# Performance work log

Measured on AMD Instinct MI355X. Metric: run time of the kernel, lower is better.

## Reference

```python
import jax, jax.numpy as jnp
import numpy as np

N_HEADS = 8
WINDOW = 4

def setup_inputs() -> dict:
    key = jax.random.key(0)
    ks = jax.random.split(key, 12)
    B, C, L = 8, 512, 1024
    Dh = C // N_HEADS
    s = 1.0 / np.sqrt(C)
    inp = {
        'x': jax.random.normal(ks[0], (B, C, L), dtype=jnp.float32),
        'Wq': jax.random.normal(ks[1], (C, C), dtype=jnp.float32) * s,
        'bq': jnp.zeros((C,), dtype=jnp.float32),
        'Wk': jax.random.normal(ks[2], (C, C), dtype=jnp.float32) * s,
        'bk': jnp.zeros((C,), dtype=jnp.float32),
        'Wv': jax.random.normal(ks[3], (C, C), dtype=jnp.float32) * s,
        'bv': jnp.zeros((C,), dtype=jnp.float32),
        'Wo': jax.random.normal(ks[4], (C, C), dtype=jnp.float32) * s,
        'bo': jnp.zeros((C,), dtype=jnp.float32),
        'emb_rel_k': jax.random.normal(ks[5], (2 * WINDOW + 1, Dh), dtype=jnp.float32) * 0.02,
        'emb_rel_v': jax.random.normal(ks[6], (2 * WINDOW + 1, Dh), dtype=jnp.float32) * 0.02,
    }
    return inp


def reference(x, Wq, bq, Wk, bk, Wv, bv, Wo, bo, emb_rel_k, emb_rel_v):
    B, C, L = x.shape
    H = N_HEADS
    Dh = C // H
    scale = Dh ** -0.5

    def proj(W, b):
        # pointwise conv1d == channel-mixing matmul; (B,C,L) -> (B,H,L,Dh)
        y = jnp.einsum('oc,bcl->bol', W, x) + b[:, None]
        return y.reshape(B, H, Dh, L).transpose(0, 1, 3, 2)

    q = proj(Wq, bq) * scale
    k = proj(Wk, bk)
    v = proj(Wv, bv)

    scores = jnp.einsum('bhld,bhjd->bhlj', q, k)  # (B,H,L,L)

    t = jnp.arange(L)
    diff = t[None, :] - t[:, None]                      # (L,L)
    window_mask = (jnp.abs(diff) <= WINDOW)
    indices = jnp.clip(diff, -WINDOW, WINDOW) + WINDOW  # (L,L) in [0, 2w]

    rel_k = emb_rel_k[indices]                          # (L,L,Dh)
    rel_scores = jnp.einsum('bhld,ljd->bhlj', q, rel_k)
    scores = scores + rel_scores * window_mask[None, None, :, :]

    attn = jax.nn.softmax(scores, axis=-1)

    out = jnp.einsum('bhlj,bhjd->bhld', attn, v)
    rel_v = emb_rel_v[indices] * window_mask[:, :, None]  # (L,L,Dh)
    out = out + jnp.einsum('bhlj,ljd->bhld', attn, rel_v)

    out = out.transpose(0, 1, 3, 2).reshape(B, C, L)
    out = jnp.einsum('oc,bcl->bol', Wo, out) + bo[:, None]
    return out
```

## Files before the change

kernel.cpp:

```cpp
#include <hip/hip_runtime.h>
#include <math.h>

#define B_  8
#define H_  8
#define C_  512
#define L_  1024
#define DH  64
#define WIN 4

typedef __attribute__((ext_vector_type(8))) short short8;
typedef __attribute__((ext_vector_type(4))) float floatx4;

__device__ __forceinline__ unsigned short f2bf(float f) {
    unsigned int u = __float_as_uint(f);
    u = u + 0x7FFFu + ((u >> 16) & 1u);
    return (unsigned short)(u >> 16);
}
__device__ __forceinline__ float bf2f(unsigned short h) {
    return __uint_as_float(((unsigned int)h) << 16);
}
__device__ __forceinline__ unsigned short f2h(float f) {
    _Float16 h = (_Float16)f;
    return *reinterpret_cast<unsigned short*>(&h);
}

__device__ __forceinline__ void gload_lds16(const void* g, void* l) {
    __builtin_amdgcn_global_load_lds(
        (const __attribute__((address_space(1))) void*)g,
        (__attribute__((address_space(3))) void*)l, 16, 0, 0);
}

__global__ __launch_bounds__(256) void prep_kernel(
    const float* __restrict__ Wq, const float* __restrict__ Wk,
    const float* __restrict__ Wv, const float* __restrict__ Wo,
    const float* __restrict__ bq, const float* __restrict__ bk,
    const float* __restrict__ bv,
    unsigned short* __restrict__ Wqkv_hi,
    unsigned short* __restrict__ Wo_h,
    float* __restrict__ bqkv)
{
    const int i = blockIdx.x * 256 + threadIdx.x;
    float4 v; ushort4 h;

    v = ((const float4*)Wq)[i];
    h.x = f2bf(v.x); h.y = f2bf(v.y); h.z = f2bf(v.z); h.w = f2bf(v.w);
    ((ushort4*)Wqkv_hi)[i] = h;

    v = ((const float4*)Wk)[i];
    h.x = f2bf(v.x); h.y = f2bf(v.y); h.z = f2bf(v.z); h.w = f2bf(v.w);
    ((ushort4*)Wqkv_hi)[65536 + i] = h;

    v = ((const float4*)Wv)[i];
    h.x = f2bf(v.x); h.y = f2bf(v.y); h.z = f2bf(v.z); h.w = f2bf(v.w);
    ((ushort4*)Wqkv_hi)[131072 + i] = h;

    v = ((const float4*)Wo)[i];
    h.x = f2h(v.x); h.y = f2h(v.y); h.z = f2h(v.z); h.w = f2h(v.w);
    ((ushort4*)Wo_h)[i] = h;

    if (i < 512)       bqkv[i] = bq[i];
    else if (i < 1024) bqkv[i] = bk[i - 512];
    else if (i < 1536) bqkv[i] = bv[i - 1024];
}

__global__ __launch_bounds__(256) void transpose_kernel(
    const float* __restrict__ x, unsigned short* __restrict__ xT)
{
    __shared__ float tile[32][33];
    const int b  = blockIdx.z;
    const int cb = blockIdx.y * 32;
    const int lb = blockIdx.x * 32;
    const int t  = threadIdx.x;
    {
        const int l = t & 31, c0 = t >> 5;
#pragma unroll
        for (int p = 0; p < 4; ++p) {
            const int c = c0 + 8 * p;
            tile[c][l] = x[((size_t)b * C_ + cb + c) * L_ + lb + l];
        }
    }
    __syncthreads();
    {
        const int c = t & 31, l0 = t >> 5;
#pragma unroll
        for (int p = 0; p < 4; ++p) {
            const int l = l0 + 8 * p;
            xT[((size_t)b * L_ + lb + l) * C_ + cb + c] = f2bf(tile[c][l]);
        }
    }
}

__global__ __launch_bounds__(256) void qkv_gemm_kernel(
    const unsigned short* __restrict__ Wh, const float* __restrict__ bqkv,
    const unsigned short* __restrict__ xT,
    unsigned short* __restrict__ Qb, unsigned short* __restrict__ Kb,
    unsigned short* __restrict__ Vc)
{
    __shared__ __align__(16) unsigned short SM[18432];

    const int b   = blockIdx.z;
    const int oB  = blockIdx.y * 128;
    const int mat = oB >> 9;
    const int ob  = oB & 511;
    const int lb  = blockIdx.x * 128;
    const int t  = threadIdx.x;
    const int w = t >> 6, lane = t & 63, quad = lane >> 4, lc = lane & 15;
    const int wm = w >> 1, wn = w & 1;

    const unsigned short* Wm = Wh + (size_t)mat * C_ * C_;

    floatx4 acc[4][4];
#pragma unroll
    for (int i = 0; i < 4; ++i)
#pragma unroll
        for (int j = 0; j < 4; ++j) acc[i][j] = (floatx4)0.f;

    const int srow = w * 32 + (lane >> 2);
    const int sc8  = (lane & 3) * 8;

#define QKV_STAGE(BUF, S) {                                                  \
    const int c0_ = (S) * 32;                                                \
    _Pragma("unroll")                                                        \
    for (int p_ = 0; p_ < 2; ++p_) {                                         \
        gload_lds16(&Wm[(size_t)(ob + srow + 16 * p_) * C_ + c0_ + sc8],     \
                    &SM[(0 * 2 + (BUF)) * 4096 + (w * 32 + p_ * 16) * 32]);  \
        gload_lds16(&xT[((size_t)b * L_ + lb + srow + 16 * p_) * C_ + c0_ + sc8], \
                    &SM[(1 * 2 + (BUF)) * 4096 + (w * 32 + p_ * 16) * 32]);  \
    }                                                                        \
}

    QKV_STAGE(0, 0)
    __syncthreads();

    for (int s = 0; s < 16; ++s) {
        const int cur = s & 1;
        if (s < 15) QKV_STAGE(1 - cur, s + 1)

        const unsigned short (*At)[32] =
            reinterpret_cast<const unsigned short (*)[32]>(&SM[(0 * 2 + cur) * 4096]);
        const unsigned short (*Bt)[32] =
            reinterpret_cast<const unsigned short (*)[32]>(&SM[(1 * 2 + cur) * 4096]);

        short8 a[4], bb[4];
#pragma unroll
        for (int mt = 0; mt < 4; ++mt)
            a[mt] = *reinterpret_cast<const short8*>(&At[wm * 64 + mt * 16 + lc][quad * 8]);
#pragma unroll
        for (int nt = 0; nt < 4; ++nt)
            bb[nt] = *reinterpret_cast<const short8*>(&Bt[wn * 64 + nt * 16 + lc][quad * 8]);
#pragma unroll
        for (int mt = 0; mt < 4; ++mt)
#pragma unroll
            for (int nt = 0; nt < 4; ++nt)
                acc[mt][nt] = __builtin_amdgcn_mfma_f32_16x16x32_bf16(
                    a[mt], bb[nt], acc[mt][nt], 0, 0, 0);

        __syncthreads();
    }

    if (mat == 2) {
#pragma unroll
        for (int mt = 0; mt < 4; ++mt) {
#pragma unroll
            for (int r = 0; r < 4; ++r) {
                const int o  = ob + wm * 64 + mt * 16 + quad * 4 + r;
                const float bi = bqkv[1024 + o];
#pragma unroll
                for (int nt = 0; nt < 4; ++nt) {
                    const int l = lb + wn * 64 + nt * 16 + lc;
                    Vc[((size_t)b * C_ + o) * L_ + l] = f2bf(acc[mt][nt][r] + bi);
                }
            }
        }
    } else {
        const float scale = (mat == 0) ? 0.125f : 1.0f;
        unsigned short* dst = (mat == 0) ? Qb : Kb;
        unsigned short (*sT)[144] =
            reinterpret_cast<unsigned short (*)[144]>(&SM[0]);

#pragma unroll
        for (int mt = 0; mt < 4; ++mt) {
#pragma unroll
            for (int r = 0; r < 4; ++r) {
                const int o  = ob + wm * 64 + mt * 16 + quad * 4 + r;
                const float bi = bqkv[mat * 512 + o];
                const int d  = mt * 16 + quad * 4 + r;
#pragma unroll
                for (int nt = 0; nt < 4; ++nt) {
                    const int l = wn * 64 + nt * 16 + lc;
                    sT[l][wm * 72 + d] = f2bf((acc[mt][nt][r] + bi) * scale);
                }
            }
        }
        __syncthreads();
        {
            const int l = t >> 1, hf = t & 1;
#pragma unroll
            for (int h01 = 0; h01 < 2; ++h01) {
                const int hgl = (ob >> 6) + h01;
                const size_t o = (((size_t)b * H_ + hgl) * L_ + lb + l) * DH + hf * 32;
                const int cbase = h01 * 72 + hf * 32;
                uint4 v0 = *reinterpret_cast<const uint4*>(&sT[l][cbase]);
                uint4 v1 = *reinterpret_cast<const uint4*>(&sT[l][cbase + 8]);
                uint4 v2 = *reinterpret_cast<const uint4*>(&sT[l][cbase + 16]);
                uint4 v3 = *reinterpret_cast<const uint4*>(&sT[l][cbase + 24]);
                *reinterpret_cast<uint4*>(&dst[o])      = v0;
                *reinterpret_cast<uint4*>(&dst[o + 8])  = v1;
                *reinterpret_cast<uint4*>(&dst[o + 16]) = v2;
                *reinterpret_cast<uint4*>(&dst[o + 24]) = v3;
            }
        }
    }
}

__global__ __launch_bounds__(256, 2) void attn_kernel15(
    const unsigned short* __restrict__ Qb,
    const unsigned short* __restrict__ Kb,
    const unsigned short* __restrict__ Vc,
    const float* __restrict__ erel_k, const float* __restrict__ erel_v,
    unsigned short* __restrict__ AOh)
{
    __shared__ __align__(16) unsigned short kst[2][64][68];
    __shared__ __align__(16) unsigned short vst[2][64][68];
    __shared__ __align__(16) unsigned short Pl[4][2][16][68];
    __shared__ float rs[128][9];
    __shared__ float rv[128][9];

    const int t  = threadIdx.x;
    const int bh = blockIdx.x;
    const int rt = blockIdx.y;
    const int b = bh >> 3, h = bh & 7;
    const int w = t >> 6, lane = t & 63, quad = lane >> 4, lc = lane & 15;
    const int rowB = rt * 128 + w * 32;

    const size_t qkBase = (size_t)bh * L_ * DH;
    const size_t vBase  = ((size_t)b * C_ + h * DH) * L_;

    for (int i = lane; i < 32 * 9; i += 64) rv[w * 32 + i / 9][i % 9] = 0.f;

    short8 af0[2], af1[2];
#pragma unroll
    for (int kk = 0; kk < 2; ++kk) {
        af0[kk] = *reinterpret_cast<const short8*>(
            &Qb[qkBase + (size_t)(rowB + lc) * DH + kk * 32 + quad * 8]);
        af1[kk] = *reinterpret_cast<const short8*>(
            &Qb[qkBase + (size_t)(rowB + 16 + lc) * DH + kk * 32 + quad * 8]);
    }

    {
        floatx4 rsa0 = (floatx4)0.f, rsa1 = (floatx4)0.f;
        const int drow = (lc < 9) ? lc : 8;
#pragma unroll
        for (int kk = 0; kk < 2; ++kk) {
            short8 bfr;
#pragma unroll
            for (int i = 0; i < 8; ++i)
                bfr[i] = (short)f2bf(erel_k[drow * 64 + kk * 32 + quad * 8 + i]);
            rsa0 = __builtin_amdgcn_mfma_f32_16x16x32_bf16(af0[kk], bfr, rsa0, 0, 0, 0);
            rsa1 = __builtin_amdgcn_mfma_f32_16x16x32_bf16(af1[kk], bfr, rsa1, 0, 0, 0);
        }
        if (lc < 9) {
#pragma unroll
            for (int r = 0; r < 4; ++r) {
                rs[w * 32 + quad * 4 + r][lc]      = rsa0[r];
                rs[w * 32 + 16 + quad * 4 + r][lc] = rsa1[r];
            }
        }
    }

    const int jr = t >> 2, jcE = (t & 3) * 16;
    *reinterpret_cast<uint4*>(&kst[0][jr][jcE]) =
        *reinterpret_cast<const uint4*>(&Kb[qkBase + (size_t)jr * DH + jcE]);
    *reinterpret_cast<uint4*>(&kst[0][jr][jcE + 8]) =
        *reinterpret_cast<const uint4*>(&Kb[qkBase + (size_t)jr * DH + jcE + 8]);
    *reinterpret_cast<uint4*>(&vst[0][jr][jcE]) =
        *reinterpret_cast<const uint4*>(&Vc[vBase + (size_t)jr * L_ + jcE]);
    *reinterpret_cast<uint4*>(&vst[0][jr][jcE + 8]) =
        *reinterpret_cast<const uint4*>(&Vc[vBase + (size_t)jr * L_ + jcE + 8]);
    __syncthreads();

    short8 ones;
#pragma unroll
    for (int j = 0; j < 8; ++j) ones[j] = (short)0x3F80;

    floatx4 acc_o0[4], acc_o1[4], acc_l0 = (floatx4)0.f, acc_l1 = (floatx4)0.f;
#pragma unroll
    for (int nt = 0; nt < 4; ++nt) { acc_o0[nt] = (floatx4)0.f; acc_o1[nt] = (floatx4)0.f; }

    for (int jt = 0; jt < L_ / 64; ++jt) {
        const int j0  = jt * 64;
        const int cur = jt & 1;

        uint4 pk0, pk1, pv0, pv1;
        if (jt < L_ / 64 - 1) {
            const int j0n = j0 + 64;
            pk0 = *reinterpret_cast<const uint4*>(
                &Kb[qkBase + (size_t)(j0n + jr) * DH + jcE]);
            pk1 = *reinterpret_cast<const uint4*>(
                &Kb[qkBase + (size_t)(j0n + jr) * DH + jcE + 8]);
            pv0 = *reinterpret_cast<const uint4*>(
                &Vc[vBase + (size_t)jr * L_ + j0n + jcE]);
            pv1 = *reinterpret_cast<const uint4*>(
                &Vc[vBase + (size_t)jr * L_ + j0n + jcE + 8]);
        }

        floatx4 s0[4], s1[4];
#pragma unroll
        for (int nt = 0; nt < 4; ++nt) { s0[nt] = (floatx4)0.f; s1[nt] = (floatx4)0.f; }
        __builtin_amdgcn_s_setprio(1);
#pragma unroll
        for (int nt = 0; nt < 4; ++nt)
#pragma unroll
            for (int kk = 0; kk < 2; ++kk) {
                const short8 kf = *reinterpret_cast<const short8*>(
                    &kst[cur][nt * 16 + lc][kk * 32 + quad * 8]);
                s0[nt] = __builtin_amdgcn_mfma_f32_16x16x32_bf16(kf, af0[kk], s0[nt], 0, 0, 0);
                s1[nt] = __builtin_amdgcn_mfma_f32_16x16x32_bf16(kf, af1[kk], s1[nt], 0, 0, 0);
            }
        __builtin_amdgcn_s_setprio(0);

        short8 pf0[2], pf1[2];

        {
            const int rowW = rowB;
            const bool nearD = (j0 <= rowW + 15 + WIN) && (j0 + 63 >= rowW - WIN);
            if (nearD) {
#pragma unroll
                for (int nt = 0; nt < 4; ++nt)
#pragma unroll
                    for (int r = 0; r < 4; ++r) {
                        const int diff = (j0 + nt * 16 + quad * 4 + r) - (rowW + lc);
                        if (diff >= -WIN && diff <= WIN)
                            s0[nt][r] += rs[w * 32 + lc][diff + WIN];
                    }
            }
#pragma unroll
            for (int nt = 0; nt < 4; ++nt) {
                const float e0 = __expf(s0[nt][0]);
                const float e1 = __expf(s0[nt][1]);
                const float e2 = __expf(s0[nt][2]);
                const float e3 = __expf(s0[nt][3]);
                unsigned int u01, u23;
                asm volatile("v_cvt_pk_bf16_f32 %0, %1, %2" : "=v"(u01) : "v"(e0), "v"(e1));
                asm volatile("v_cvt_pk_bf16_f32 %0, %1, %2" : "=v"(u23) : "v"(e2), "v"(e3));
                uint2 pr; pr.x = u01; pr.y = u23;
                *reinterpret_cast<uint2*>(&Pl[w][0][lc][nt * 16 + quad * 4]) = pr;
            }
            if (nearD) {
                for (int idx = lane; idx < 16 * 9; idx += 64) {
                    const int r16 = idx / 9, dr = idx % 9;
                    const int jg = rowW + r16 + dr - WIN;
                    if (jg >= j0 && jg < j0 + 64 && jg >= 0 && jg < L_)
                        rv[w * 32 + r16][dr] += bf2f(Pl[w][0][r16][jg - j0]);
                }
            }
#pragma unroll
            for (int kk = 0; kk < 2; ++kk)
                pf0[kk] = *reinterpret_cast<const short8*>(&Pl[w][0][lc][kk * 32 + quad * 8]);
        }

        {
            const int rowW = rowB + 16;
            const bool nearD = (j0 <= rowW + 15 + WIN) && (j0 + 63 >= rowW - WIN);
            if (nearD) {
#pragma unroll
                for (int nt = 0; nt < 4; ++nt)
#pragma unroll
                    for (int r = 0; r < 4; ++r) {
                        const int diff = (j0 + nt * 16 + quad * 4 + r) - (rowW + lc);
                        if (diff >= -WIN && diff <= WIN)
                            s1[nt][r] += rs[w * 32 + 16 + lc][diff + WIN];
                    }
            }
#pragma unroll
            for (int nt = 0; nt < 4; ++nt) {
                const float e0 = __expf(s1[nt][0]);
                const float e1 = __expf(s1[nt][1]);
                const float e2 = __expf(s1[nt][2]);
                const float e3 = __expf(s1[nt][3]);
                unsigned int u01, u23;
                asm volatile("v_cvt_pk_bf16_f32 %0, %1, %2" : "=v"(u01) : "v"(e0), "v"(e1));
                asm volatile("v_cvt_pk_bf16_f32 %0, %1, %2" : "=v"(u23) : "v"(e2), "v"(e3));
                uint2 pr; pr.x = u01; pr.y = u23;
                *reinterpret_cast<uint2*>(&Pl[w][1][lc][nt * 16 + quad * 4]) = pr;
            }
            if (nearD) {
                for (int idx = lane; idx < 16 * 9; idx += 64) {
                    const int r16 = idx / 9, dr = idx % 9;
                    const int jg = rowW + r16 + dr - WIN;
                    if (jg >= j0 && jg < j0 + 64 && jg >= 0 && jg < L_)
                        rv[w * 32 + 16 + r16][dr] += bf2f(Pl[w][1][r16][jg - j0]);
                }
            }
#pragma unroll
            for (int kk = 0; kk < 2; ++kk)
                pf1[kk] = *reinterpret_cast<const short8*>(&Pl[w][1][lc][kk * 32 + quad * 8]);
        }

        __builtin_amdgcn_s_setprio(1);
#pragma unroll
        for (int kk = 0; kk < 2; ++kk) {
            acc_l0 = __builtin_amdgcn_mfma_f32_16x16x32_bf16(pf0[kk], ones, acc_l0, 0, 0, 0);
            acc_l1 = __builtin_amdgcn_mfma_f32_16x16x32_bf16(pf1[kk], ones, acc_l1, 0, 0, 0);
        }
#pragma unroll
        for (int nt = 0; nt < 4; ++nt)
#pragma unroll
            for (int kk = 0; kk < 2; ++kk) {
                const short8 vf = *reinterpret_cast<const short8*>(
                    &vst[cur][nt * 16 + lc][kk * 32 + quad * 8]);
                acc_o0[nt] = __builtin_amdgcn_mfma_f32_16x16x32_bf16(pf0[kk], vf, acc_o0[nt], 0, 0, 0);
                acc_o1[nt] = __builtin_amdgcn_mfma_f32_16x16x32_bf16(pf1[kk], vf, acc_o1[nt], 0, 0, 0);
            }
        __builtin_amdgcn_s_setprio(0);

        if (jt < L_ / 64 - 1) {
            *reinterpret_cast<uint4*>(&kst[1 - cur][jr][jcE])     = pk0;
            *reinterpret_cast<uint4*>(&kst[1 - cur][jr][jcE + 8]) = pk1;
            *reinterpret_cast<uint4*>(&vst[1 - cur][jr][jcE])     = pv0;
            *reinterpret_cast<uint4*>(&vst[1 - cur][jr][jcE + 8]) = pv1;
        }
        __syncthreads();
    }

    {
#pragma unroll
        for (int nt = 0; nt < 4; ++nt) {
            const int d = nt * 16 + lc;
            float ev[9];
#pragma unroll
            for (int dr = 0; dr < 9; ++dr) ev[dr] = erel_v[dr * 64 + d];
#pragma unroll
            for (int r = 0; r < 4; ++r) {
                const int rloc = w * 32 + quad * 4 + r;
                float v = acc_o0[nt][r];
#pragma unroll
                for (int dr = 0; dr < 9; ++dr) v += rv[rloc][dr] * ev[dr];
                Pl[w][0][quad * 4 + r][nt * 16 + lc] = f2h(v / acc_l0[r]);
            }
        }
        const int row = lane >> 2, ds8 = (lane & 3) * 16;
        const uint4 q0 = *reinterpret_cast<const uint4*>(&Pl[w][0][row][ds8]);
        const uint4 q1 = *reinterpret_cast<const uint4*>(&Pl[w][0][row][ds8 + 8]);
        const size_t o = ((size_t)b * L_ + rowB + row) * C_ + h * 64 + ds8;
        *reinterpret_cast<uint4*>(&AOh[o])     = q0;
        *reinterpret_cast<uint4*>(&AOh[o + 8]) = q1;
    }
    {
#pragma unroll
        for (int nt = 0; nt < 4; ++nt) {
            const int d = nt * 16 + lc;
            float ev[9];
#pragma unroll
            for (int dr = 0; dr < 9; ++dr) ev[dr] = erel_v[dr * 64 + d];
#pragma unroll
            for (int r = 0; r < 4; ++r) {
                const int rloc = w * 32 + 16 + quad * 4 + r;
                float v = acc_o1[nt][r];
#pragma unroll
                for (int dr = 0; dr < 9; ++dr) v += rv[rloc][dr] * ev[dr];
                Pl[w][1][quad * 4 + r][nt * 16 + lc] = f2h(v / acc_l1[r]);
            }
        }
        const int row = lane >> 2, ds8 = (lane & 3) * 16;
        const uint4 q0 = *reinterpret_cast<const uint4*>(&Pl[w][1][row][ds8]);
        const uint4 q1 = *reinterpret_cast<const uint4*>(&Pl[w][1][row][ds8 + 8]);
        const size_t o = ((size_t)b * L_ + rowB + 16 + row) * C_ + h * 64 + ds8;
        *reinterpret_cast<uint4*>(&AOh[o])     = q0;
        *reinterpret_cast<uint4*>(&AOh[o + 8]) = q1;
    }
}

__global__ __launch_bounds__(256) void out_gemm_kernel(
    const unsigned short* __restrict__ Wh,
    const float* __restrict__ bo,
    const unsigned short* __restrict__ Ah,
    float* __restrict__ Y)
{
    __shared__ __align__(16) unsigned short Asb[2][128][32];
    __shared__ __align__(16) unsigned short Bsb[2][64][32];

    const int b  = blockIdx.z;
    const int ob = blockIdx.y * 128;
    const int lb = blockIdx.x * 64;
    const int t  = threadIdx.x;
    const int w = t >> 6, lane = t & 63, quad = lane >> 4, lc = lane & 15;
    const int wm = w >> 1, wn = w & 1;

    floatx4 acc[4][2];
#pragma unroll
    for (int i = 0; i < 4; ++i)
#pragma unroll
        for (int j = 0; j < 2; ++j) acc[i][j] = (floatx4)0.f;

    const int srow = (lane >> 2);
    const int sc8  = (lane & 3) * 8;

#define OG_STAGE(BUF, S) {                                                   \
    const int c0_ = (S) * 32;                                                \
    _Pragma("unroll")                                                        \
    for (int p_ = 0; p_ < 2; ++p_)                                           \
        gload_lds16(&Wh[(size_t)(ob + w * 32 + p_ * 16 + srow) * C_ + c0_ + sc8], \
                    &Asb[BUF][w * 32 + p_ * 16][0]);                         \
    gload_lds16(&Ah[((size_t)b * L_ + lb + w * 16 + srow) * C_ + c0_ + sc8], \
                &Bsb[BUF][w * 16][0]);                                       \
}

    OG_STAGE(0, 0)
    __syncthreads();

    for (int s = 0; s < 16; ++s) {
        const int cur = s & 1;
        if (s < 15) OG_STAGE(1 - cur, s + 1)

        short8 ah[4], bhf[2];
#pragma unroll
        for (int mt = 0; mt < 4; ++mt)
            ah[mt] = *reinterpret_cast<const short8*>(
                &Asb[cur][wm * 64 + mt * 16 + lc][quad * 8]);
#pragma unroll
        for (int nt = 0; nt < 2; ++nt)
            bhf[nt] = *reinterpret_cast<const short8*>(
                &Bsb[cur][wn * 32 + nt * 16 + lc][quad * 8]);
#pragma unroll
        for (int mt = 0; mt < 4; ++mt)
#pragma unroll
            for (int nt = 0; nt < 2; ++nt)
                acc[mt][nt] = __builtin_amdgcn_mfma_f32_16x16x32_f16(
                    ah[mt], bhf[nt], acc[mt][nt], 0, 0, 0);

        __syncthreads();
    }

#pragma unroll
    for (int mt = 0; mt < 4; ++mt) {
#pragma unroll
        for (int r = 0; r < 4; ++r) {
            const int o = ob + wm * 64 + mt * 16 + quad * 4 + r;
            const float bi = bo[o];
#pragma unroll
            for (int nt = 0; nt < 2; ++nt) {
                const int l = lb + wn * 32 + nt * 16 + lc;
                Y[((size_t)b * C_ + o) * L_ + l] = acc[mt][nt][r] + bi;
            }
        }
    }
}

extern "C" void kernel_launch(void* const* d_in, const int* in_sizes, int n_in,
                              void* d_out, int out_size, void* d_ws, size_t ws_size,
                              hipStream_t stream)
{
    const float* x   = (const float*)d_in[0];
    const float* Wq  = (const float*)d_in[1];
    const float* bq  = (const float*)d_in[2];
    const float* Wk  = (const float*)d_in[3];
    const float* bk  = (const float*)d_in[4];
    const float* Wv  = (const float*)d_in[5];
    const float* bv  = (const float*)d_in[6];
    const float* Wo  = (const float*)d_in[7];
    const float* bo  = (const float*)d_in[8];
    const float* erk = (const float*)d_in[9];
    const float* erv = (const float*)d_in[10];

    char* ws = (char*)d_ws;
    const size_t MB = 1024u * 1024u;
    unsigned short* xT      = (unsigned short*)(ws);
    unsigned short* Qb      = (unsigned short*)(ws + 8 * MB);
    unsigned short* Kb      = (unsigned short*)(ws + 16 * MB);
    unsigned short* Vc      = (unsigned short*)(ws + 24 * MB);
    unsigned short* AOh     = (unsigned short*)(ws + 32 * MB);
    unsigned short* Wqkv_hi = (unsigned short*)(ws + 40 * MB);
    unsigned short* Wo_h    = (unsigned short*)(ws + 42 * MB);
    float*          bqkv    = (float*)(ws + 43 * MB);

    prep_kernel<<<256, 256, 0, stream>>>(Wq, Wk, Wv, Wo, bq, bk, bv,
                                         Wqkv_hi, Wo_h, bqkv);
    transpose_kernel<<<dim3(L_ / 32, C_ / 32, B_), 256, 0, stream>>>(x, xT);
    qkv_gemm_kernel<<<dim3(L_ / 128, 12, B_), 256, 0, stream>>>(
        Wqkv_hi, bqkv, xT, Qb, Kb, Vc);
    attn_kernel15<<<dim3(64, 8), 256, 0, stream>>>(
        Qb, Kb, Vc, erk, erv, AOh);
    out_gemm_kernel<<<dim3(L_ / 64, C_ / 128, B_), 256, 0, stream>>>(
        Wo_h, bo, AOh, (float*)d_out);
}
```

Measured before the change: 164.3 us.

## Merge prep and transpose kernels; use two-wave QKV GEMM blocks with larger per-wave tiles

The weight-conversion kernel and the x transpose kernel become one launch that dispatches on block index, saving a kernel launch and its inter-kernel gap. The QKV GEMM drops from 4 to 2 waves per 128x128 block. Each wave now computes a 64x128 tile with 32 accumulators, which raises B-fragment reuse and cuts LDS reads per MFMA. In exchange each wave uses more registers, and there are fewer waves to hide load latency.

```diff
diff --git a/kernel.cpp b/kernel.cpp
--- a/kernel.cpp
+++ b/kernel.cpp
@@ -30,67 +30,69 @@
         (__attribute__((address_space(3))) void*)l, 16, 0, 0);
 }
 
-__global__ __launch_bounds__(256) void prep_kernel(
+__global__ __launch_bounds__(256) void prep_transpose_kernel(
+    const float* __restrict__ x,
     const float* __restrict__ Wq, const float* __restrict__ Wk,
     const float* __restrict__ Wv, const float* __restrict__ Wo,
     const float* __restrict__ bq, const float* __restrict__ bk,
     const float* __restrict__ bv,
+    unsigned short* __restrict__ xT,
     unsigned short* __restrict__ Wqkv_hi,
     unsigned short* __restrict__ Wo_h,
     float* __restrict__ bqkv)
 {
-    const int i = blockIdx.x * 256 + threadIdx.x;
-    float4 v; ushort4 h;
-
-    v = ((const float4*)Wq)[i];
-    h.x = f2bf(v.x); h.y = f2bf(v.y); h.z = f2bf(v.z); h.w = f2bf(v.w);
-    ((ushort4*)Wqkv_hi)[i] = h;
-
-    v = ((const float4*)Wk)[i];
-    h.x = f2bf(v.x); h.y = f2bf(v.y); h.z = f2bf(v.z); h.w = f2bf(v.w);
-    ((ushort4*)Wqkv_hi)[65536 + i] = h;
-
-    v = ((const float4*)Wv)[i];
-    h.x = f2bf(v.x); h.y = f2bf(v.y); h.z = f2bf(v.z); h.w = f2bf(v.w);
-    ((ushort4*)Wqkv_hi)[131072 + i] = h;
-
-    v = ((const float4*)Wo)[i];
-    h.x = f2h(v.x); h.y = f2h(v.y); h.z = f2h(v.z); h.w = f2h(v.w);
-    ((ushort4*)Wo_h)[i] = h;
-
-    if (i < 512)       bqkv[i] = bq[i];
-    else if (i < 1024) bqkv[i] = bk[i - 512];
-    else if (i < 1536) bqkv[i] = bv[i - 1024];
-}
-
-__global__ __launch_bounds__(256) void transpose_kernel(
-    const float* __restrict__ x, unsigned short* __restrict__ xT)
-{
     __shared__ float tile[32][33];
-    const int b  = blockIdx.z;
-    const int cb = blockIdx.y * 32;
-    const int lb = blockIdx.x * 32;
-    const int t  = threadIdx.x;
-    {
-        const int l = t & 31, c0 = t >> 5;
-#pragma unroll
-        for (int p = 0; p < 4; ++p) {
-            const int c = c0 + 8 * p;
-            tile[c][l] = x[((size_t)b * C_ + cb + c) * L_ + lb + l];
-        }
-    }
-    __syncthreads();
-    {
-        const int c = t & 31, l0 = t >> 5;
-#pragma unroll
-        for (int p = 0; p < 4; ++p) {
-            const int l = l0 + 8 * p;
-            xT[((size_t)b * L_ + lb + l) * C_ + cb + c] = f2bf(tile[c][l]);
-        }
-    }
-}
-
-__global__ __launch_bounds__(256) void qkv_gemm_kernel(
+    const int bid = blockIdx.x;
+    const int t   = threadIdx.x;
+
+    if (bid < 4096) {
+        const int b  = bid >> 9;
+        const int cb = ((bid >> 5) & 15) * 32;
+        const int lb = (bid & 31) * 32;
+        {
+            const int l = t & 31, c0 = t >> 5;
+#pragma unroll
+            for (int p = 0; p < 4; ++p) {
+                const int c = c0 + 8 * p;
+                tile[c][l] = x[((size_t)b * C_ + cb + c) * L_ + lb + l];
+            }
+        }
+        __syncthreads();
+        {
+            const int c = t & 31, l0 = t >> 5;
+#pragma unroll
+            for (int p = 0; p < 4; ++p) {
+                const int l = l0 + 8 * p;
+                xT[((size_t)b * L_ + lb + l) * C_ + cb + c] = f2bf(tile[c][l]);
+            }
+        }
+    } else {
+        const int i = (bid - 4096) * 256 + t;
+        float4 v; ushort4 h;
+
+        v = ((const float4*)Wq)[i];
+        h.x = f2bf(v.x); h.y = f2bf(v.y); h.z = f2bf(v.z); h.w = f2bf(v.w);
+        ((ushort4*)Wqkv_hi)[i] = h;
+
+        v = ((const float4*)Wk)[i];
+        h.x = f2bf(v.x); h.y = f2bf(v.y); h.z = f2bf(v.z); h.w = f2bf(v.w);
+        ((ushort4*)Wqkv_hi)[65536 + i] = h;
+
+        v = ((const float4*)Wv)[i];
+        h.x = f2bf(v.x); h.y = f2bf(v.y); h.z = f2bf(v.z); h.w = f2bf(v.w);
+        ((ushort4*)Wqkv_hi)[131072 + i] = h;
+
+        v = ((const float4*)Wo)[i];
+        h.x = f2h(v.x); h.y = f2h(v.y); h.z = f2h(v.z); h.w = f2h(v.w);
+        ((ushort4*)Wo_h)[i] = h;
+
+        if (i < 512)       bqkv[i] = bq[i];
+        else if (i < 1024) bqkv[i] = bk[i - 512];
+        else if (i < 1536) bqkv[i] = bv[i - 1024];
+    }
+}
+
+__global__ __launch_bounds__(128) void qkv_gemm_kernel(
     const unsigned short* __restrict__ Wh, const float* __restrict__ bqkv,
     const unsigned short* __restrict__ xT,
     unsigned short* __restrict__ Qb, unsigned short* __restrict__ Kb,
@@ -105,27 +107,28 @@
     const int lb  = blockIdx.x * 128;
     const int t  = threadIdx.x;
     const int w = t >> 6, lane = t & 63, quad = lane >> 4, lc = lane & 15;
-    const int wm = w >> 1, wn = w & 1;
 
     const unsigned short* Wm = Wh + (size_t)mat * C_ * C_;
 
-    floatx4 acc[4][4];
+    floatx4 acc[4][8];
 #pragma unroll
     for (int i = 0; i < 4; ++i)
 #pragma unroll
-        for (int j = 0; j < 4; ++j) acc[i][j] = (floatx4)0.f;
-
-    const int srow = w * 32 + (lane >> 2);
+        for (int j = 0; j < 8; ++j) acc[i][j] = (floatx4)0.f;
+
+    const int srow = (lane >> 2);
     const int sc8  = (lane & 3) * 8;
 
 #define QKV_STAGE(BUF, S) {                                                  \
     const int c0_ = (S) * 32;                                                \
     _Pragma("unroll")                                                        \
-    for (int p_ = 0; p_ < 2; ++p_) {                                         \
-        gload_lds16(&Wm[(size_t)(ob + srow + 16 * p_) * C_ + c0_ + sc8],     \
-                    &SM[(0 * 2 + (BUF)) * 4096 + (w * 32 + p_ * 16) * 32]);  \
-        gload_lds16(&xT[((size_t)b * L_ + lb + srow + 16 * p_) * C_ + c0_ + sc8], \
-                    &SM[(1 * 2 + (BUF)) * 4096 + (w * 32 + p_ * 16) * 32]);  \
+    for (int i_ = 0; i_ < 4; ++i_) {                                         \
+        const int ck_ = w * 4 + i_;                                          \
+        const int r0_ = ck_ * 16 + srow;                                     \
+        gload_lds16(&Wm[(size_t)(ob + r0_) * C_ + c0_ + sc8],                \
+                    &SM[(0 * 2 + (BUF)) * 4096 + ck_ * 512]);                \
+        gload_lds16(&xT[((size_t)b * L_ + lb + r0_) * C_ + c0_ + sc8],       \
+                    &SM[(1 * 2 + (BUF)) * 4096 + ck_ * 512]);                \
     }                                                                        \
 }
 
@@ -141,17 +144,17 @@
         const unsigned short (*Bt)[32] =
             reinterpret_cast<const unsigned short (*)[32]>(&SM[(1 * 2 + cur) * 4096]);
 
-        short8 a[4], bb[4];
+        short8 a[4], bb[8];
 #pragma unroll
         for (int mt = 0; mt < 4; ++mt)
-            a[mt] = *reinterpret_cast<const short8*>(&At[wm * 64 + mt * 16 + lc][quad * 8]);
-#pragma unroll
-        for (int nt = 0; nt < 4; ++nt)
-            bb[nt] = *reinterpret_cast<const short8*>(&Bt[wn * 64 + nt * 16 + lc][quad * 8]);
+            a[mt] = *reinterpret_cast<const short8*>(&At[w * 64 + mt * 16 + lc][quad * 8]);
+#pragma unroll
+        for (int nt = 0; nt < 8; ++nt)
+            bb[nt] = *reinterpret_cast<const short8*>(&Bt[nt * 16 + lc][quad * 8]);
 #pragma unroll
         for (int mt = 0; mt < 4; ++mt)
 #pragma unroll
-            for (int nt = 0; nt < 4; ++nt)
+            for (int nt = 0; nt < 8; ++nt)
                 acc[mt][nt] = __builtin_amdgcn_mfma_f32_16x16x32_bf16(
                     a[mt], bb[nt], acc[mt][nt], 0, 0, 0);
 
@@ -163,11 +166,11 @@
         for (int mt = 0; mt < 4; ++mt) {
 #pragma unroll
             for (int r = 0; r < 4; ++r) {
-                const int o  = ob + wm * 64 + mt * 16 + quad * 4 + r;
+                const int o  = ob + w * 64 + mt * 16 + quad * 4 + r;
                 const float bi = bqkv[1024 + o];
 #pragma unroll
-                for (int nt = 0; nt < 4; ++nt) {
-                    const int l = lb + wn * 64 + nt * 16 + lc;
+                for (int nt = 0; nt < 8; ++nt) {
+                    const int l = lb + nt * 16 + lc;
                     Vc[((size_t)b * C_ + o) * L_ + l] = f2bf(acc[mt][nt][r] + bi);
                 }
             }
@@ -182,32 +185,36 @@
         for (int mt = 0; mt < 4; ++mt) {
 #pragma unroll
             for (int r = 0; r < 4; ++r) {
-                const int o  = ob + wm * 64 + mt * 16 + quad * 4 + r;
+                const int o  = ob + w * 64 + mt * 16 + quad * 4 + r;
                 const float bi = bqkv[mat * 512 + o];
                 const int d  = mt * 16 + quad * 4 + r;
 #pragma unroll
-                for (int nt = 0; nt < 4; ++nt) {
-                    const int l = wn * 64 + nt * 16 + lc;
-                    sT[l][wm * 72 + d] = f2bf((acc[mt][nt][r] + bi) * scale);
+                for (int nt = 0; nt < 8; ++nt) {
+                    const int l = nt * 16 + lc;
+                    sT[l][w * 72 + d] = f2bf((acc[mt][nt][r] + bi) * scale);
                 }
             }
         }
         __syncthreads();
         {
-            const int l = t >> 1, hf = t & 1;
-#pragma unroll
-            for (int h01 = 0; h01 < 2; ++h01) {
-                const int hgl = (ob >> 6) + h01;
-                const size_t o = (((size_t)b * H_ + hgl) * L_ + lb + l) * DH + hf * 32;
-                const int cbase = h01 * 72 + hf * 32;
-                uint4 v0 = *reinterpret_cast<const uint4*>(&sT[l][cbase]);
-                uint4 v1 = *reinterpret_cast<const uint4*>(&sT[l][cbase + 8]);
-                uint4 v2 = *reinterpret_cast<const uint4*>(&sT[l][cbase + 16]);
-                uint4 v3 = *reinterpret_cast<const uint4*>(&sT[l][cbase + 24]);
-                *reinterpret_cast<uint4*>(&dst[o])      = v0;
-                *reinterpret_cast<uint4*>(&dst[o + 8])  = v1;
-                *reinterpret_cast<uint4*>(&dst[o + 16]) = v2;
-                *reinterpret_cast<uint4*>(&dst[o + 24]) = v3;
+            const int hf = t & 1;
+#pragma unroll
+            for (int lh = 0; lh < 2; ++lh) {
+                const int l = lh * 64 + (t >> 1);
+#pragma unroll
+                for (int h01 = 0; h01 < 2; ++h01) {
+                    const int hgl = (ob >> 6) + h01;
+                    const size_t o = (((size_t)b * H_ + hgl) * L_ + lb + l) * DH + hf * 32;
+                    const int cbase = h01 * 72 + hf * 32;
+                    uint4 v0 = *reinterpret_cast<const uint4*>(&sT[l][cbase]);
+                    uint4 v1 = *reinterpret_cast<const uint4*>(&sT[l][cbase + 8]);
+                    uint4 v2 = *reinterpret_cast<const uint4*>(&sT[l][cbase + 16]);
+                    uint4 v3 = *reinterpret_cast<const uint4*>(&sT[l][cbase + 24]);
+                    *reinterpret_cast<uint4*>(&dst[o])      = v0;
+                    *reinterpret_cast<uint4*>(&dst[o + 8])  = v1;
+                    *reinterpret_cast<uint4*>(&dst[o + 16]) = v2;
+                    *reinterpret_cast<uint4*>(&dst[o + 24]) = v3;
+                }
             }
         }
     }
@@ -574,10 +581,9 @@
     unsigned short* Wo_h    = (unsigned short*)(ws + 42 * MB);
     float*          bqkv    = (float*)(ws + 43 * MB);
 
-    prep_kernel<<<256, 256, 0, stream>>>(Wq, Wk, Wv, Wo, bq, bk, bv,
-                                         Wqkv_hi, Wo_h, bqkv);
-    transpose_kernel<<<dim3(L_ / 32, C_ / 32, B_), 256, 0, stream>>>(x, xT);
-    qkv_gemm_kernel<<<dim3(L_ / 128, 12, B_), 256, 0, stream>>>(
+    prep_transpose_kernel<<<4352, 256, 0, stream>>>(
+        x, Wq, Wk, Wv, Wo, bq, bk, bv, xT, Wqkv_hi, Wo_h, bqkv);
+    qkv_gemm_kernel<<<dim3(L_ / 128, 12, B_), 128, 0, stream>>>(
         Wqkv_hi, bqkv, xT, Qb, Kb, Vc);
     attn_kernel15<<<dim3(64, 8), 256, 0, stream>>>(
         Qb, Kb, Vc, erk, erv, AOh);
```

Result: slower. 171.4 us (+4.3%).
